# Performance work log

Measured on AMD Instinct MI355X. Metric: run time of the kernel, lower is better.

## Reference

```python
import jax, jax.numpy as jnp
import numpy as np

D_MODEL = 1024
D_HEAD = 64


def setup_inputs() -> dict:
    key = jax.random.key(0)
    k_x, k_q, k_k, k_v, k_o = jax.random.split(key, 5)
    scale = 1.0 / np.sqrt(D_MODEL)
    residual_stream = jax.random.normal(k_x, (4, 2048, D_MODEL), dtype=jnp.float32)
    Q = scale * jax.random.normal(k_q, (D_MODEL, D_HEAD), dtype=jnp.float32)
    K = scale * jax.random.normal(k_k, (D_MODEL, D_HEAD), dtype=jnp.float32)
    V = scale * jax.random.normal(k_v, (D_MODEL, D_HEAD), dtype=jnp.float32)
    O = scale * jax.random.normal(k_o, (D_MODEL, D_HEAD), dtype=jnp.float32)
    return {"residual_stream": residual_stream, "Q": Q, "K": K, "V": V, "O": O}


def reference(residual_stream, Q, K, V, O) -> jnp.ndarray:
    # queries/keys: [B, S, d_head]
    queries = jnp.einsum('bsd,dh->bsh', residual_stream, Q)
    keys = jnp.einsum('bsd,dh->bsh', residual_stream, K)
    # NOTE: original module applies NO 1/sqrt(d_head) scaling.
    pre_attention = jnp.einsum('bqh,bkh->bqk', queries, keys)  # [B, S, S]
    S = pre_attention.shape[-1]
    causal = jnp.tril(jnp.ones((S, S), dtype=bool))
    pre_attention = jnp.where(causal[None], pre_attention, -jnp.inf)
    attention = jax.nn.softmax(pre_attention, axis=-1)
    # x = residual @ V @ O^T : [B, S, d_model]
    x = jnp.einsum('bsd,dh,eh->bse', residual_stream, V, O)
    return jnp.einsum('bqk,bke->bqe', attention, x)
```

## Files before the change

### kernel.cpp

```cpp
#include <hip/hip_runtime.h>
#include <hip/hip_bf16.h>
#include <math.h>

#define BATCH 4
#define SEQ   2048
#define DM    1024
#define DH    64
#define NROWS (BATCH*SEQ)

typedef __hip_bfloat16 bf16;
typedef __attribute__((ext_vector_type(8))) short short8;
typedef __attribute__((ext_vector_type(4))) float floatx4;

__device__ __forceinline__ ushort f2bf(float f) {
    union { bf16 h; ushort u; } cv;
    cv.h = __float2bfloat16(f);
    return cv.u;
}
__device__ __forceinline__ float bf2f(ushort u) {
    union { unsigned int i; float f; } v; v.i = ((unsigned int)u) << 16; return v.f;
}

__device__ __forceinline__ void load_lds16(const ushort* g, ushort* l) {
    __builtin_amdgcn_global_load_lds(
        (const __attribute__((address_space(1))) unsigned int*)g,
        (__attribute__((address_space(3))) unsigned int*)l, 16, 0, 0);
}

__global__ __launch_bounds__(256) void wprep_kernel(
    const float* __restrict__ Q, const float* __restrict__ K,
    const float* __restrict__ V, ushort* __restrict__ WhT, ushort* __restrict__ WlT)
{
    int n = blockIdx.x;
    const float* W = (n < 64) ? Q : (n < 128) ? K : V;
    int c = n & 63;
    for (int k = threadIdx.x; k < DM; k += 256) {
        float w = W[k * DH + c];
        ushort hi = f2bf(w);
        WhT[n * DM + k] = hi;
        WlT[n * DM + k] = f2bf(w - bf2f(hi));
    }
}

__global__ __launch_bounds__(256) void qkv_part_kernel(
    const float* __restrict__ x, const ushort* __restrict__ WhT,
    const ushort* __restrict__ WlT, float* __restrict__ Cpart)
{
    __shared__ __align__(16) ushort Xs[2][32][34];
    __shared__ __align__(16) ushort Ws[2][192][34];
    int s0 = blockIdx.x * 32;
    int kb = blockIdx.y * 256;
    int t = threadIdx.x;
    int wave = t >> 6, lane = t & 63, m_ = lane & 15, qd = lane >> 4;
    const floatx4 z4 = {0.f, 0.f, 0.f, 0.f};
    floatx4 accq[2] = {z4, z4}, acck[2] = {z4, z4}, accv[2] = {z4, z4};
    int xr = t >> 3, xc = (t & 7) * 4;
    for (int k0 = 0; k0 < 256; k0 += 32) {
        float4 v = *(const float4*)&x[(size_t)(s0 + xr) * DM + kb + k0 + xc];
        ushort h0 = f2bf(v.x), h1 = f2bf(v.y), h2 = f2bf(v.z), h3 = f2bf(v.w);
        *(ushort4*)&Xs[0][xr][xc] = make_ushort4(h0, h1, h2, h3);
        *(ushort4*)&Xs[1][xr][xc] = make_ushort4(
            f2bf(v.x - bf2f(h0)), f2bf(v.y - bf2f(h1)),
            f2bf(v.z - bf2f(h2)), f2bf(v.w - bf2f(h3)));
        #pragma unroll
        for (int j = 0; j < 3; ++j) {
            int idx = t + j * 256, n = idx >> 2, kc = (idx & 3) * 8;
            *(uint4*)&Ws[0][n][kc] = *(const uint4*)&WhT[n * DM + kb + k0 + kc];
            *(uint4*)&Ws[1][n][kc] = *(const uint4*)&WlT[n * DM + kb + k0 + kc];
        }
        __syncthreads();
        short8 ah[2], al[2];
        #pragma unroll
        for (int mi = 0; mi < 2; ++mi) {
            ah[mi] = *(const short8*)&Xs[0][mi * 16 + m_][qd * 8];
            al[mi] = *(const short8*)&Xs[1][mi * 16 + m_][qd * 8];
        }
        int nq = wave * 16 + m_, nk = 64 + wave * 16 + m_, nv = 128 + wave * 16 + m_;
        short8 bqh = *(const short8*)&Ws[0][nq][qd * 8];
        short8 bql = *(const short8*)&Ws[1][nq][qd * 8];
        short8 bkh = *(const short8*)&Ws[0][nk][qd * 8];
        short8 bkl = *(const short8*)&Ws[1][nk][qd * 8];
        short8 bvh = *(const short8*)&Ws[0][nv][qd * 8];
        #pragma unroll
        for (int mi = 0; mi < 2; ++mi) {
            accq[mi] = __builtin_amdgcn_mfma_f32_16x16x32_bf16(ah[mi], bqh, accq[mi], 0, 0, 0);
            accq[mi] = __builtin_amdgcn_mfma_f32_16x16x32_bf16(al[mi], bqh, accq[mi], 0, 0, 0);
            accq[mi] = __builtin_amdgcn_mfma_f32_16x16x32_bf16(ah[mi], bql, accq[mi], 0, 0, 0);
            acck[mi] = __builtin_amdgcn_mfma_f32_16x16x32_bf16(ah[mi], bkh, acck[mi], 0, 0, 0);
            acck[mi] = __builtin_amdgcn_mfma_f32_16x16x32_bf16(al[mi], bkh, acck[mi], 0, 0, 0);
            acck[mi] = __builtin_amdgcn_mfma_f32_16x16x32_bf16(ah[mi], bkl, acck[mi], 0, 0, 0);
            accv[mi] = __builtin_amdgcn_mfma_f32_16x16x32_bf16(ah[mi], bvh, accv[mi], 0, 0, 0);
        }
        __syncthreads();
    }
    float* Cp = Cpart + (size_t)blockIdx.y * (NROWS * 192);
    #pragma unroll
    for (int mi = 0; mi < 2; ++mi) {
        #pragma unroll
        for (int r = 0; r < 4; ++r) {
            int row = s0 + mi * 16 + qd * 4 + r;
            float* base = Cp + (size_t)row * 192;
            base[wave * 16 + m_]       = accq[mi][r];
            base[64 + wave * 16 + m_]  = acck[mi][r];
            base[128 + wave * 16 + m_] = accv[mi][r];
        }
    }
}

__global__ __launch_bounds__(256) void qkv_reduce_kernel(
    const float* __restrict__ Cpart,
    ushort* __restrict__ qh, ushort* __restrict__ ql,
    ushort* __restrict__ kh, ushort* __restrict__ kl, ushort* __restrict__ xvh)
{
    const size_t SL = (size_t)NROWS * 192;
    int row0 = blockIdx.x * 8;
    int t = threadIdx.x;
    #pragma unroll
    for (int i = 0; i < 6; ++i) {
        int e = i * 256 + t;
        int r = e / 192, c = e - r * 192;
        size_t row = row0 + r;
        size_t off = row * 192 + c;
        float s = Cpart[off] + Cpart[SL + off] + Cpart[2 * SL + off] + Cpart[3 * SL + off];
        ushort hi = f2bf(s);
        ushort lo = f2bf(s - bf2f(hi));
        if (c < 64) {
            qh[row * 64 + c] = hi; ql[row * 64 + c] = lo;
        } else if (c < 128) {
            kh[row * 64 + c - 64] = hi; kl[row * 64 + c - 64] = lo;
        } else {
            xvh[row * 64 + c - 128] = hi;
        }
    }
}

__global__ __launch_bounds__(256) void xvo_kernel(
    const ushort* __restrict__ xvh, const float* __restrict__ O, ushort* __restrict__ xvoT)
{
    __shared__ __align__(16) ushort As[64 * 72];
    __shared__ __align__(16) ushort Bs[64 * 72];
    int e0 = blockIdx.x << 6;
    int row0 = blockIdx.y << 6;
    int t = threadIdx.x;
    int tr = t >> 2, tc = (t & 3) << 4;
    {
        const float* s1 = O + (size_t)(e0 + tr) * DH + tc;
        #pragma unroll
        for (int j = 0; j < 4; ++j) {
            float4 v1 = *(const float4*)(s1 + j * 4);
            uint2 w1;
            w1.x = (uint)f2bf(v1.x) | ((uint)f2bf(v1.y) << 16);
            w1.y = (uint)f2bf(v1.z) | ((uint)f2bf(v1.w) << 16);
            *(uint2*)&As[tr * 72 + tc + j * 4] = w1;
        }
        *(uint4*)&Bs[tr * 72 + tc]     = *(const uint4*)&xvh[(size_t)(row0 + tr) * DH + tc];
        *(uint4*)&Bs[tr * 72 + tc + 8] = *(const uint4*)&xvh[(size_t)(row0 + tr) * DH + tc + 8];
    }
    __syncthreads();
    int wave = t >> 6, lane = t & 63, m_ = lane & 15, qd = lane >> 4;
    const floatx4 z4 = {0.f, 0.f, 0.f, 0.f};
    floatx4 acc[4] = {z4, z4, z4, z4};
    #pragma unroll
    for (int k0 = 0; k0 < 64; k0 += 32) {
        short8 a = *(const short8*)&As[(wave * 16 + m_) * 72 + k0 + qd * 8];
        #pragma unroll
        for (int ni = 0; ni < 4; ++ni) {
            short8 bfr = *(const short8*)&Bs[(ni * 16 + m_) * 72 + k0 + qd * 8];
            acc[ni] = __builtin_amdgcn_mfma_f32_16x16x32_bf16(a, bfr, acc[ni], 0, 0, 0);
        }
    }
    int b = row0 >> 11, sl = row0 & 2047;
    #pragma unroll
    for (int r = 0; r < 4; ++r) {
        int e = e0 + wave * 16 + qd * 4 + r;
        ushort* orow = xvoT + (((size_t)(b * DM + e)) << 11) + sl;
        #pragma unroll
        for (int ni = 0; ni < 4; ++ni)
            orow[ni * 16 + m_] = f2bf(acc[ni][r]);
    }
}

__global__ __launch_bounds__(512) void softmax_kernel(
    const ushort* __restrict__ qh, const ushort* __restrict__ ql,
    const ushort* __restrict__ kh, const ushort* __restrict__ kl,
    ushort* __restrict__ P, float* __restrict__ linv)
{
    __shared__ __align__(16) ushort Qs[2][32][72];
    __shared__ float lred[8][32];
    int s0g = blockIdx.x * 32;
    int b = s0g >> 11;
    int srow = s0g & 2047;
    int t = threadIdx.x, wave = t >> 6, lane = t & 63, m_ = lane & 15, qd = lane >> 4;
    if (t < 256) {
        int r = t >> 3, c = (t & 7) * 8;
        *(uint4*)&Qs[0][r][c] = *(const uint4*)&qh[(size_t)(s0g + r) * 64 + c];
        *(uint4*)&Qs[1][r][c] = *(const uint4*)&ql[(size_t)(s0g + r) * 64 + c];
    }
    __syncthreads();
    const ushort* khb = kh + ((size_t)b << 11) * 64;
    const ushort* klb = kl + ((size_t)b << 11) * 64;
    int ntiles = ((srow + 31) >> 6) + 1;
    const floatx4 z4 = {0.f, 0.f, 0.f, 0.f};
    float lloc[2][4] = {{0.f, 0.f, 0.f, 0.f}, {0.f, 0.f, 0.f, 0.f}};
    for (int ti = wave; ti < ntiles; ti += 8) {
        int k0 = ti << 6;
        floatx4 acc[2][4];
        #pragma unroll
        for (int mi = 0; mi < 2; ++mi)
            #pragma unroll
            for (int ni = 0; ni < 4; ++ni) acc[mi][ni] = z4;
        #pragma unroll
        for (int kk = 0; kk < 2; ++kk) {
            short8 ah0 = *(const short8*)&Qs[0][0 * 16 + m_][kk * 32 + qd * 8];
            short8 ah1 = *(const short8*)&Qs[0][1 * 16 + m_][kk * 32 + qd * 8];
            short8 al0 = *(const short8*)&Qs[1][0 * 16 + m_][kk * 32 + qd * 8];
            short8 al1 = *(const short8*)&Qs[1][1 * 16 + m_][kk * 32 + qd * 8];
            #pragma unroll
            for (int ni = 0; ni < 4; ++ni) {
                size_t koff = (size_t)(k0 + ni * 16 + m_) * 64 + kk * 32 + qd * 8;
                short8 bh = *(const short8*)&khb[koff];
                short8 bl = *(const short8*)&klb[koff];
                acc[0][ni] = __builtin_amdgcn_mfma_f32_16x16x32_bf16(ah0, bh, acc[0][ni], 0, 0, 0);
                acc[0][ni] = __builtin_amdgcn_mfma_f32_16x16x32_bf16(al0, bh, acc[0][ni], 0, 0, 0);
                acc[0][ni] = __builtin_amdgcn_mfma_f32_16x16x32_bf16(ah0, bl, acc[0][ni], 0, 0, 0);
                acc[1][ni] = __builtin_amdgcn_mfma_f32_16x16x32_bf16(ah1, bh, acc[1][ni], 0, 0, 0);
                acc[1][ni] = __builtin_amdgcn_mfma_f32_16x16x32_bf16(al1, bh, acc[1][ni], 0, 0, 0);
                acc[1][ni] = __builtin_amdgcn_mfma_f32_16x16x32_bf16(ah1, bl, acc[1][ni], 0, 0, 0);
            }
        }
        #pragma unroll
        for (int mi = 0; mi < 2; ++mi)
            #pragma unroll
            for (int ni = 0; ni < 4; ++ni) {
                int kc = k0 + ni * 16 + m_;
                #pragma unroll
                for (int r = 0; r < 4; ++r) {
                    int row = srow + mi * 16 + qd * 4 + r;
                    float p = (kc <= row) ? __expf(acc[mi][ni][r]) : 0.f;
                    lloc[mi][r] += p;
                    P[(size_t)(s0g + mi * 16 + qd * 4 + r) * 2048 + kc] = f2bf(p);
                }
            }
    }
    #pragma unroll
    for (int d = 1; d < 16; d <<= 1)
        #pragma unroll
        for (int mi = 0; mi < 2; ++mi)
            #pragma unroll
            for (int r = 0; r < 4; ++r)
                lloc[mi][r] += __shfl_xor(lloc[mi][r], d);
    if (m_ == 0)
        #pragma unroll
        for (int mi = 0; mi < 2; ++mi)
            #pragma unroll
            for (int r = 0; r < 4; ++r)
                lred[wave][mi * 16 + qd * 4 + r] = lloc[mi][r];
    __syncthreads();
    if (t < 32) {
        float s = 0.f;
        #pragma unroll
        for (int w = 0; w < 8; ++w) s += lred[w][t];
        linv[s0g + t] = 1.f / s;
    }
}

__global__ __launch_bounds__(256) void av_kernel(
    const ushort* __restrict__ P, const ushort* __restrict__ xvoT,
    float* __restrict__ out, const float* __restrict__ linv)
{
    __shared__ __align__(16) ushort As[64 * 32];
    __shared__ __align__(16) ushort Bs[128 * 32];
    int bid = blockIdx.x;
    int my = 31 - (bid >> 5);
    int r5 = bid & 31;
    int b = r5 & 3;
    int n0 = (r5 >> 2) << 7;
    int m0 = my << 6;
    int t = threadIdx.x, wave = t >> 6, lane = t & 63, m_ = lane & 15, qd = lane >> 4;
    const ushort* Pb = P + ((size_t)b << 22);
    const ushort* Xb = xvoT + ((size_t)(b * DM) << 11);
    const floatx4 z4 = {0.f, 0.f, 0.f, 0.f};
    floatx4 acc[2][4];
    #pragma unroll
    for (int mi = 0; mi < 2; ++mi)
        #pragma unroll
        for (int ni = 0; ni < 4; ++ni) acc[mi][ni] = z4;
    int mb = (wave >> 1) << 5;
    int nb = (wave & 1) << 6;
    int lrow = lane >> 2;
    int gch = (((lane & 3) ^ ((lane >> 3) & 3)) << 3);
    int swz = (m_ >> 1) & 3;
    int k_end = m0 + 64;
    for (int k0 = 0; k0 < k_end; k0 += 32) {
        #pragma unroll
        for (int i = 0; i < 3; ++i) {
            int c = wave * 3 + i;
            if (c < 4)
                load_lds16(Pb + (size_t)(m0 + c * 16 + lrow) * SEQ + k0 + gch, &As[c * 16 * 32]);
            else {
                int cb = c - 4;
                load_lds16(Xb + (size_t)(n0 + cb * 16 + lrow) * SEQ + k0 + gch, &Bs[cb * 16 * 32]);
            }
        }
        __syncthreads();
        short8 a[2], bb[4];
        #pragma unroll
        for (int mi = 0; mi < 2; ++mi)
            a[mi] = *(const short8*)&As[(mb + mi * 16 + m_) * 32 + ((qd ^ swz) << 3)];
        #pragma unroll
        for (int ni = 0; ni < 4; ++ni)
            bb[ni] = *(const short8*)&Bs[(nb + ni * 16 + m_) * 32 + ((qd ^ swz) << 3)];
        #pragma unroll
        for (int mi = 0; mi < 2; ++mi)
            #pragma unroll
            for (int ni = 0; ni < 4; ++ni)
                acc[mi][ni] = __builtin_amdgcn_mfma_f32_16x16x32_bf16(a[mi], bb[ni], acc[mi][ni], 0, 0, 0);
        __syncthreads();
    }
    float* ob = out + (size_t)b * SEQ * DM;
    const float* lb = linv + ((size_t)b << 11);
    #pragma unroll
    for (int mi = 0; mi < 2; ++mi) {
        #pragma unroll
        for (int r = 0; r < 4; ++r) {
            int row = m0 + mb + mi * 16 + qd * 4 + r;
            float scale = lb[row];
            float* orow = ob + (size_t)row * DM + n0 + nb;
            #pragma unroll
            for (int ni = 0; ni < 4; ++ni)
                orow[ni * 16 + m_] = acc[mi][ni][r] * scale;
        }
    }
}

extern "C" void kernel_launch(void* const* d_in, const int* in_sizes, int n_in,
                              void* d_out, int out_size, void* d_ws, size_t ws_size,
                              hipStream_t stream) {
    const float* x = (const float*)d_in[0];
    const float* Q = (const float*)d_in[1];
    const float* K = (const float*)d_in[2];
    const float* V = (const float*)d_in[3];
    const float* O = (const float*)d_in[4];
    float* out = (float*)d_out;

    char* ws = (char*)d_ws;
    ushort* qh   = (ushort*)(ws);
    ushort* ql   = (ushort*)(ws + (1ull  << 20));
    ushort* kh   = (ushort*)(ws + (2ull  << 20));
    ushort* kl   = (ushort*)(ws + (3ull  << 20));
    ushort* xvh  = (ushort*)(ws + (4ull  << 20));
    ushort* WhT  = (ushort*)(ws + (5ull  << 20));
    ushort* WlT  = (ushort*)(ws + (5ull  << 20) + (512ull << 10));
    float*  linv = (float*) (ws + (6ull  << 20));
    ushort* xvoT = (ushort*)(ws + (7ull  << 20));
    ushort* Pbuf = (ushort*)(ws + (23ull << 20));
    float*  Cpart = (float*)(ws + (23ull << 20));

    wprep_kernel<<<192, 256, 0, stream>>>(Q, K, V, WhT, WlT);
    qkv_part_kernel<<<dim3(NROWS / 32, 4), 256, 0, stream>>>(x, WhT, WlT, Cpart);
    qkv_reduce_kernel<<<NROWS / 8, 256, 0, stream>>>(Cpart, qh, ql, kh, kl, xvh);
    xvo_kernel<<<dim3(DM / 64, NROWS / 64), 256, 0, stream>>>(xvh, O, xvoT);
    softmax_kernel<<<NROWS / 32, 512, 0, stream>>>(qh, ql, kh, kl, Pbuf, linv);
    av_kernel<<<32 * 8 * 4, 256, 0, stream>>>(Pbuf, xvoT, out, linv);
}
```

Before: 185.3 us.

## Split softmax key tiles across two blocks and double-buffer AV kernel loads

The softmax kernel now runs twice as many blocks, each handling every other 64-key tile, and writes partial row sums that the AV kernel adds and inverts at the end. The AV kernel's K step grows from 32 to 64 and uses a double-buffered LDS pipeline with an XOR swizzle, so the next tile's async global-to-LDS loads are issued before the current tile's MFMAs. The aim is more parallelism for the short causal rows and fewer barriers with load latency hidden behind compute. The cost is more LDS per block (48KB), which may lower occupancy, plus one extra partial-sum read per output row.

```diff
diff --git a/kernel.cpp b/kernel.cpp
--- a/kernel.cpp
+++ b/kernel.cpp
@@ -183,11 +183,12 @@
 __global__ __launch_bounds__(512) void softmax_kernel(
     const ushort* __restrict__ qh, const ushort* __restrict__ ql,
     const ushort* __restrict__ kh, const ushort* __restrict__ kl,
-    ushort* __restrict__ P, float* __restrict__ linv)
+    ushort* __restrict__ P, float* __restrict__ lpart)
 {
     __shared__ __align__(16) ushort Qs[2][32][72];
     __shared__ float lred[8][32];
     int s0g = blockIdx.x * 32;
+    int split = blockIdx.y;
     int b = s0g >> 11;
     int srow = s0g & 2047;
     int t = threadIdx.x, wave = t >> 6, lane = t & 63, m_ = lane & 15, qd = lane >> 4;
@@ -202,7 +203,7 @@
     int ntiles = ((srow + 31) >> 6) + 1;
     const floatx4 z4 = {0.f, 0.f, 0.f, 0.f};
     float lloc[2][4] = {{0.f, 0.f, 0.f, 0.f}, {0.f, 0.f, 0.f, 0.f}};
-    for (int ti = wave; ti < ntiles; ti += 8) {
+    for (int ti = 2 * wave + split; ti < ntiles; ti += 16) {
         int k0 = ti << 6;
         floatx4 acc[2][4];
         #pragma unroll
@@ -260,16 +261,16 @@
         float s = 0.f;
         #pragma unroll
         for (int w = 0; w < 8; ++w) s += lred[w][t];
-        linv[s0g + t] = 1.f / s;
+        lpart[split * NROWS + s0g + t] = s;
     }
 }
 
 __global__ __launch_bounds__(256) void av_kernel(
     const ushort* __restrict__ P, const ushort* __restrict__ xvoT,
-    float* __restrict__ out, const float* __restrict__ linv)
-{
-    __shared__ __align__(16) ushort As[64 * 32];
-    __shared__ __align__(16) ushort Bs[128 * 32];
+    float* __restrict__ out, const float* __restrict__ lpart)
+{
+    __shared__ __align__(16) ushort As[2][64 * 64];
+    __shared__ __align__(16) ushort Bs[2][128 * 64];
     int bid = blockIdx.x;
     int my = 31 - (bid >> 5);
     int r5 = bid & 31;
@@ -287,44 +288,58 @@
         for (int ni = 0; ni < 4; ++ni) acc[mi][ni] = z4;
     int mb = (wave >> 1) << 5;
     int nb = (wave & 1) << 6;
-    int lrow = lane >> 2;
-    int gch = (((lane & 3) ^ ((lane >> 3) & 3)) << 3);
-    int swz = (m_ >> 1) & 3;
-    int k_end = m0 + 64;
-    for (int k0 = 0; k0 < k_end; k0 += 32) {
-        #pragma unroll
-        for (int i = 0; i < 3; ++i) {
-            int c = wave * 3 + i;
-            if (c < 4)
-                load_lds16(Pb + (size_t)(m0 + c * 16 + lrow) * SEQ + k0 + gch, &As[c * 16 * 32]);
-            else {
-                int cb = c - 4;
-                load_lds16(Xb + (size_t)(n0 + cb * 16 + lrow) * SEQ + k0 + gch, &Bs[cb * 16 * 32]);
+    int drow = lane >> 3;
+    int dlc = ((lane & 7) ^ drow) << 3;
+    int ntk = my + 1;
+    #define AV_STAGE(ti, buf)                                                   \
+        {                                                                       \
+            int k0_ = (ti) << 6;                                                \
+            _Pragma("unroll")                                                   \
+            for (int i_ = 0; i_ < 6; ++i_) {                                    \
+                int c_ = wave * 6 + i_;                                         \
+                if (c_ < 8)                                                     \
+                    load_lds16(Pb + (size_t)(m0 + c_ * 8 + drow) * SEQ + k0_ + dlc, \
+                               &As[buf][c_ * 512]);                             \
+                else                                                            \
+                    load_lds16(Xb + (size_t)(n0 + (c_ - 8) * 8 + drow) * SEQ + k0_ + dlc, \
+                               &Bs[buf][(c_ - 8) * 512]);                       \
+            }                                                                   \
+        }
+    AV_STAGE(0, 0)
+    for (int ti = 0; ti < ntk; ++ti) {
+        __syncthreads();
+        if (ti + 1 < ntk) AV_STAGE(ti + 1, (ti + 1) & 1)
+        int bufi = ti & 1;
+        short8 a[2][2], bb[2][4];
+        #pragma unroll
+        for (int kk = 0; kk < 2; ++kk) {
+            #pragma unroll
+            for (int mi = 0; mi < 2; ++mi) {
+                int row = mb + mi * 16 + m_;
+                a[kk][mi] = *(const short8*)&As[bufi][row * 64 + (((kk << 2) + qd) ^ (row & 7)) * 8];
             }
-        }
-        __syncthreads();
-        short8 a[2], bb[4];
-        #pragma unroll
-        for (int mi = 0; mi < 2; ++mi)
-            a[mi] = *(const short8*)&As[(mb + mi * 16 + m_) * 32 + ((qd ^ swz) << 3)];
-        #pragma unroll
-        for (int ni = 0; ni < 4; ++ni)
-            bb[ni] = *(const short8*)&Bs[(nb + ni * 16 + m_) * 32 + ((qd ^ swz) << 3)];
-        #pragma unroll
-        for (int mi = 0; mi < 2; ++mi)
-            #pragma unroll
-            for (int ni = 0; ni < 4; ++ni)
-                acc[mi][ni] = __builtin_amdgcn_mfma_f32_16x16x32_bf16(a[mi], bb[ni], acc[mi][ni], 0, 0, 0);
-        __syncthreads();
+            #pragma unroll
+            for (int ni = 0; ni < 4; ++ni) {
+                int row = nb + ni * 16 + m_;
+                bb[kk][ni] = *(const short8*)&Bs[bufi][row * 64 + (((kk << 2) + qd) ^ (row & 7)) * 8];
+            }
+        }
+        #pragma unroll
+        for (int kk = 0; kk < 2; ++kk)
+            #pragma unroll
+            for (int mi = 0; mi < 2; ++mi)
+                #pragma unroll
+                for (int ni = 0; ni < 4; ++ni)
+                    acc[mi][ni] = __builtin_amdgcn_mfma_f32_16x16x32_bf16(a[kk][mi], bb[kk][ni], acc[mi][ni], 0, 0, 0);
     }
     float* ob = out + (size_t)b * SEQ * DM;
-    const float* lb = linv + ((size_t)b << 11);
     #pragma unroll
     for (int mi = 0; mi < 2; ++mi) {
         #pragma unroll
         for (int r = 0; r < 4; ++r) {
             int row = m0 + mb + mi * 16 + qd * 4 + r;
-            float scale = lb[row];
+            int rowg = (b << 11) + row;
+            float scale = 1.f / (lpart[rowg] + lpart[NROWS + rowg]);
             float* orow = ob + (size_t)row * DM + n0 + nb;
             #pragma unroll
             for (int ni = 0; ni < 4; ++ni)
@@ -351,7 +366,7 @@
     ushort* xvh  = (ushort*)(ws + (4ull  << 20));
     ushort* WhT  = (ushort*)(ws + (5ull  << 20));
     ushort* WlT  = (ushort*)(ws + (5ull  << 20) + (512ull << 10));
-    float*  linv = (float*) (ws + (6ull  << 20));
+    float*  lpart = (float*)(ws + (6ull  << 20));
     ushort* xvoT = (ushort*)(ws + (7ull  << 20));
     ushort* Pbuf = (ushort*)(ws + (23ull << 20));
     float*  Cpart = (float*)(ws + (23ull << 20));
@@ -360,6 +375,6 @@
     qkv_part_kernel<<<dim3(NROWS / 32, 4), 256, 0, stream>>>(x, WhT, WlT, Cpart);
     qkv_reduce_kernel<<<NROWS / 8, 256, 0, stream>>>(Cpart, qh, ql, kh, kl, xvh);
     xvo_kernel<<<dim3(DM / 64, NROWS / 64), 256, 0, stream>>>(xvh, O, xvoT);
-    softmax_kernel<<<NROWS / 32, 512, 0, stream>>>(qh, ql, kh, kl, Pbuf, linv);
-    av_kernel<<<32 * 8 * 4, 256, 0, stream>>>(Pbuf, xvoT, out, linv);
-}
+    softmax_kernel<<<dim3(NROWS / 32, 2), 512, 0, stream>>>(qh, ql, kh, kl, Pbuf, lpart);
+    av_kernel<<<32 * 8 * 4, 256, 0, stream>>>(Pbuf, xvoT, out, lpart);
+}
```

New measurement: 177.3 us. 1.04x faster.
